# Kernel optimization log

Hardware: AMD Instinct MI355X
Metric: run time of the kernel (lower is better)

The kernel has to match this reference:

```python
import jax, jax.numpy as jnp
import numpy as np

N = 100000
E = 1600000
N_FEAT = 128
H1 = 256
H2 = 32
N_CLASS = 16


def spmm(row, col, vals, x):
    # sparse [N,N] @ dense [N,d]: gather source rows, scale by edge value,
    # scatter-add into destination rows.
    return jax.ops.segment_sum(vals[:, None] * x[col], row, num_segments=N)


def setup_inputs() -> dict:
    key = jax.random.key(0)
    ks = jax.random.split(key, 12)
    x_in = jax.random.normal(ks[0], (N, N_FEAT), dtype=jnp.float32)
    adj_row = jax.random.randint(ks[1], (E,), 0, N, dtype=jnp.int64)
    adj_col = jax.random.randint(ks[2], (E,), 0, N, dtype=jnp.int64)
    adj_vals = jax.random.uniform(ks[3], (E,), dtype=jnp.float32)
    s1 = 1.0 / np.sqrt(N_FEAT)
    s2 = 1.0 / np.sqrt(H1)
    s3 = 1.0 / np.sqrt(H2)
    W1 = jax.random.uniform(ks[4], (N_FEAT, H1), jnp.float32, -s1, s1)
    b1 = jax.random.uniform(ks[5], (H1,), jnp.float32, -s1, s1)
    W2 = jax.random.uniform(ks[6], (H1, H2), jnp.float32, -s2, s2)
    b2 = jax.random.uniform(ks[7], (H2,), jnp.float32, -s2, s2)
    W3 = jax.random.uniform(ks[8], (H2, N_CLASS), jnp.float32, -s3, s3)
    b3 = jax.random.uniform(ks[9], (N_CLASS,), jnp.float32, -s3, s3)
    return {"x_in": x_in, "adj_row": adj_row, "adj_col": adj_col,
            "adj_vals": adj_vals, "W1": W1, "b1": b1, "W2": W2, "b2": b2,
            "W3": W3, "b3": b3}


def reference(x_in, adj_row, adj_col, adj_vals, W1, b1, W2, b2, W3, b3):
    # layer 1: ReLU(Linear(adj @ x)); dropout is identity at inference
    h = jax.nn.relu(spmm(adj_row, adj_col, adj_vals, x_in) @ W1 + b1)
    # layer 2: ReLU(Linear(adj @ h))
    t = jax.nn.relu(spmm(adj_row, adj_col, adj_vals, h) @ W2 + b2)
    logits = t @ W3 + b3
    return jax.nn.log_softmax(logits, axis=1), t
```

## Files before the change

### kernel.cpp

```cpp
#include <hip/hip_runtime.h>
#include <hip/hip_bf16.h>

#define NN 100000
#define NE 1600000
#define NF 128
#define NH1 256
#define NH2 32
#define NC 16

#define NB 196
#define BSH 9
#define NCHUNK 512
#define CHSZ (NE / NCHUNK)

typedef __attribute__((ext_vector_type(4))) float f32x4;
typedef __attribute__((ext_vector_type(8))) short s16x8;
typedef __attribute__((ext_vector_type(4))) short s16x4;

__device__ __forceinline__ unsigned short f2bu(float f) {
    union { float f; unsigned u; } v; v.f = f;
    unsigned r = v.u + 0x7FFFu + ((v.u >> 16) & 1u);
    return (unsigned short)(r >> 16);
}
__device__ __forceinline__ float bflo(unsigned w) { return __uint_as_float(w << 16); }
__device__ __forceinline__ float bfhi(unsigned w) { return __uint_as_float(w & 0xFFFF0000u); }

__device__ __forceinline__ int detect_st(const int* arow) {
    const unsigned* a = (const unsigned*)arow;
    unsigned acc = 0;
#pragma unroll
    for (int i = 1; i < 32; i += 2) acc |= a[i];
    return acc == 0u ? 2 : 1;
}

__global__ __launch_bounds__(256) void fat0_k(const float* __restrict__ x, short* __restrict__ xb,
                                              const float* __restrict__ W1, const float* __restrict__ W2,
                                              short* __restrict__ w1t, short* __restrict__ w2t,
                                              const int* __restrict__ arow, int* __restrict__ histc) {
    int bid = blockIdx.x;
    if (bid < NCHUNK) {
        __shared__ int h[NB];
        for (int j = threadIdx.x; j < NB; j += 256) h[j] = 0;
        __syncthreads();
        int st = detect_st(arow);
        int base = bid * CHSZ;
        for (int i = base + threadIdx.x; i < base + CHSZ; i += 256)
            atomicAdd(&h[arow[(size_t)i * st] >> BSH], 1);
        __syncthreads();
        for (int j = threadIdx.x; j < NB; j += 256) histc[bid * NB + j] = h[j];
    } else if (bid < NCHUNK + 1024) {
        const int total = NN * NF / 4;
        for (int i = (bid - NCHUNK) * 256 + threadIdx.x; i < total; i += 1024 * 256) {
            f32x4 v = ((const f32x4*)x)[i];
            s16x4 o;
            for (int j = 0; j < 4; ++j) o[j] = (short)f2bu(v[j]);
            ((s16x4*)xb)[i] = o;
        }
    } else {
        int i = (bid - NCHUNK - 1024) * 256 + threadIdx.x;
        if (i < NF * NH1) {
            int k = i / NH1, c = i % NH1;
            w1t[c * NF + k] = (short)f2bu(W1[i]);
        } else {
            int j = i - NF * NH1;
            if (j < NH1 * NH2) {
                int k = j / NH2, c = j % NH2;
                w2t[c * NH1 + k] = (short)f2bu(W2[j]);
            }
        }
    }
}

__global__ __launch_bounds__(256) void scanb_k(const int* __restrict__ histc,
                                               int* __restrict__ cur,
                                               int* __restrict__ totals) {
    __shared__ int s[256];
    int b = blockIdx.x, t = threadIdx.x;
    int v0 = histc[(2 * t) * NB + b], v1 = histc[(2 * t + 1) * NB + b];
    int sum = v0 + v1;
    s[t] = sum; __syncthreads();
    for (int off = 1; off < 256; off <<= 1) {
        int u = (t >= off) ? s[t - off] : 0;
        __syncthreads();
        s[t] += u;
        __syncthreads();
    }
    int excl = s[t] - sum;
    cur[(2 * t) * NB + b] = excl;
    cur[(2 * t + 1) * NB + b] = excl + v0;
    if (t == 255) totals[b] = s[255];
}

__global__ __launch_bounds__(256) void scat_k(const int* __restrict__ arow,
                                              const int* __restrict__ acol,
                                              const float* __restrict__ avals,
                                              const int* __restrict__ totals,
                                              const int* __restrict__ cur,
                                              uint2* __restrict__ recs) {
    __shared__ int lcur[NB];
    __shared__ int ss[256];
    int t = threadIdx.x;
    int tv = (t < NB) ? totals[t] : 0;
    ss[t] = tv; __syncthreads();
    for (int off = 1; off < 256; off <<= 1) {
        int u = (t >= off) ? ss[t - off] : 0;
        __syncthreads();
        ss[t] += u;
        __syncthreads();
    }
    if (t < NB) lcur[t] = (ss[t] - tv) + cur[blockIdx.x * NB + t];
    __syncthreads();
    int st = detect_st(arow);
    int base = blockIdx.x * CHSZ;
    for (int i = base + t; i < base + CHSZ; i += 256) {
        int r   = arow[(size_t)i * st];
        int col = acol[(size_t)i * st];
        float v = avals[i];
        int b = r >> BSH;
        int p = atomicAdd(&lcur[b], 1);
        uint2 rec;
        rec.x = (unsigned)col | ((unsigned)(r & 511) << 17);
        rec.y = __float_as_uint(v);
        recs[p] = rec;
    }
}

__global__ __launch_bounds__(256) void sortb_k(const uint2* __restrict__ recs,
                                               const int* __restrict__ totals,
                                               int* __restrict__ rptr,
                                               uint2* __restrict__ epack) {
    __shared__ int hist[512], cur[512], sc[256], ss[256];
    __shared__ int s0sh, s1sh;
    int b = blockIdx.x, t = threadIdx.x;
    int tv = (t < NB) ? totals[t] : 0;
    ss[t] = tv; __syncthreads();
    for (int off = 1; off < 256; off <<= 1) {
        int u = (t >= off) ? ss[t - off] : 0;
        __syncthreads();
        ss[t] += u;
        __syncthreads();
    }
    if (t == b) { s0sh = ss[t] - tv; s1sh = ss[t]; }
    for (int j = t; j < 512; j += 256) hist[j] = 0;
    __syncthreads();
    int s0 = s0sh, s1 = s1sh;
    for (int i = s0 + t; i < s1; i += 256)
        atomicAdd(&hist[(recs[i].x >> 17) & 511], 1);
    __syncthreads();
    int v0 = hist[2 * t], v1 = hist[2 * t + 1], sum = v0 + v1;
    sc[t] = sum; __syncthreads();
    for (int off = 1; off < 256; off <<= 1) {
        int u = (t >= off) ? sc[t - off] : 0;
        __syncthreads();
        sc[t] += u;
        __syncthreads();
    }
    int excl = sc[t] - sum;
    cur[2 * t] = excl; cur[2 * t + 1] = excl + v0;
    __syncthreads();
    int nrows = NN - b * 512; if (nrows > 512) nrows = 512;
    for (int j = t; j < nrows; j += 256) rptr[b * 512 + j] = s0 + cur[j];
    if (b == 0 && t == 0) rptr[NN] = NE;
    __syncthreads();
    for (int i = s0 + t; i < s1; i += 256) {
        uint2 rc = recs[i];
        int rl = (rc.x >> 17) & 511;
        int p = s0 + atomicAdd(&cur[rl], 1);
        uint2 ep;
        ep.x = rc.x & 0x1FFFF;
        ep.y = rc.y;
        epack[p] = ep;
    }
}

__global__ __launch_bounds__(256) void spmm1_k(const int* __restrict__ rptr,
                                               const uint2* __restrict__ ep,
                                               const short* __restrict__ xb,
                                               short* __restrict__ agg1) {
    int row = blockIdx.x * 4 + (threadIdx.x >> 6);
    if (row >= NN) return;
    int lane = threadIdx.x & 63;
    int q = lane >> 4, f = lane & 15;
    int s = rptr[row], e = rptr[row + 1];
    float acc[8] = {};
    int i = s + q;
    for (; i + 4 < e; i += 8) {
        uint2 m0 = ep[i];
        uint2 m1 = ep[i + 4];
        uint4 g0 = *(const uint4*)&xb[(size_t)m0.x * NF + f * 8];
        uint4 g1 = *(const uint4*)&xb[(size_t)m1.x * NF + f * 8];
        float v0 = __uint_as_float(m0.y);
        float v1 = __uint_as_float(m1.y);
        acc[0] += v0 * bflo(g0.x); acc[1] += v0 * bfhi(g0.x);
        acc[2] += v0 * bflo(g0.y); acc[3] += v0 * bfhi(g0.y);
        acc[4] += v0 * bflo(g0.z); acc[5] += v0 * bfhi(g0.z);
        acc[6] += v0 * bflo(g0.w); acc[7] += v0 * bfhi(g0.w);
        acc[0] += v1 * bflo(g1.x); acc[1] += v1 * bfhi(g1.x);
        acc[2] += v1 * bflo(g1.y); acc[3] += v1 * bfhi(g1.y);
        acc[4] += v1 * bflo(g1.z); acc[5] += v1 * bfhi(g1.z);
        acc[6] += v1 * bflo(g1.w); acc[7] += v1 * bfhi(g1.w);
    }
    if (i < e) {
        uint2 m = ep[i];
        uint4 g = *(const uint4*)&xb[(size_t)m.x * NF + f * 8];
        float v = __uint_as_float(m.y);
        acc[0] += v * bflo(g.x); acc[1] += v * bfhi(g.x);
        acc[2] += v * bflo(g.y); acc[3] += v * bfhi(g.y);
        acc[4] += v * bflo(g.z); acc[5] += v * bfhi(g.z);
        acc[6] += v * bflo(g.w); acc[7] += v * bfhi(g.w);
    }
#pragma unroll
    for (int j = 0; j < 8; ++j) {
        acc[j] += __shfl_xor(acc[j], 16, 64);
        acc[j] += __shfl_xor(acc[j], 32, 64);
    }
    if (q == 0) {
        uint4 o4;
        o4.x = ((unsigned)f2bu(acc[1]) << 16) | f2bu(acc[0]);
        o4.y = ((unsigned)f2bu(acc[3]) << 16) | f2bu(acc[2]);
        o4.z = ((unsigned)f2bu(acc[5]) << 16) | f2bu(acc[4]);
        o4.w = ((unsigned)f2bu(acc[7]) << 16) | f2bu(acc[6]);
        *(uint4*)&agg1[(size_t)row * NF + f * 8] = o4;
    }
}

__global__ __launch_bounds__(256) void gemm12_k(const short* __restrict__ agg1,
                                                const short* __restrict__ w1t,
                                                const float* __restrict__ b1,
                                                const short* __restrict__ w2t,
                                                short* __restrict__ hw) {
    __shared__ char lds[87040];
    short* a_s  = (short*)lds;
    short* w_s  = (short*)(lds + 17408);
    short* h_s  = (short*)lds;
    short* w2_s = (short*)(lds + 33792);
    int tid = threadIdx.x;
    int r0 = blockIdx.x * 64;
    {
        int row = tid >> 2, kk = (tid & 3) * 32, gr = r0 + row;
        for (int i = 0; i < 4; ++i) {
            int k = kk + i * 8;
            s16x8 v = {};
            if (gr < NN) v = *(const s16x8*)&agg1[(size_t)gr * NF + k];
            *(s16x8*)&a_s[row * 136 + k] = v;
        }
    }
    {
        for (int i = 0; i < 16; ++i) {
            int k = i * 8;
            *(s16x8*)&w_s[tid * 136 + k] = *(const s16x8*)&w1t[(size_t)tid * NF + k];
        }
    }
    __syncthreads();
    int w = tid >> 6, l = tid & 63, lr = l & 15, hi = l >> 4;
    f32x4 acc[4][4] = {};
    for (int ks = 0; ks < 4; ++ks) {
        int kb = ks * 32 + hi * 8;
        s16x8 ar[4], br[4];
        for (int mi = 0; mi < 4; ++mi) ar[mi] = *(const s16x8*)&a_s[(mi * 16 + lr) * 136 + kb];
        for (int nj = 0; nj < 4; ++nj) br[nj] = *(const s16x8*)&w_s[(w * 64 + nj * 16 + lr) * 136 + kb];
        for (int mi = 0; mi < 4; ++mi)
            for (int nj = 0; nj < 4; ++nj)
                acc[mi][nj] = __builtin_amdgcn_mfma_f32_16x16x32_bf16(ar[mi], br[nj], acc[mi][nj], 0, 0, 0);
    }
    float bias[4];
    for (int nj = 0; nj < 4; ++nj) bias[nj] = b1[w * 64 + nj * 16 + lr];
    __syncthreads();
    for (int mi = 0; mi < 4; ++mi) {
        int rr = mi * 16 + hi * 4;
        for (int nj = 0; nj < 4; ++nj) {
            int cc = w * 64 + nj * 16 + lr;
            for (int q = 0; q < 4; ++q) {
                float v = acc[mi][nj][q] + bias[nj];
                v = v > 0.f ? v : 0.f;
                h_s[(rr + q) * 264 + cc] = (short)f2bu(v);
            }
        }
    }
    {
        int c = tid >> 3, kk = (tid & 7) * 32;
        for (int i = 0; i < 4; ++i) {
            int k = kk + i * 8;
            *(s16x8*)&w2_s[c * 264 + k] = *(const s16x8*)&w2t[(size_t)c * NH1 + k];
        }
    }
    __syncthreads();
    f32x4 acc2[2] = {};
    for (int ks = 0; ks < 8; ++ks) {
        int kb = ks * 32 + hi * 8;
        s16x8 ar = *(const s16x8*)&h_s[(w * 16 + lr) * 264 + kb];
        for (int nj = 0; nj < 2; ++nj) {
            s16x8 br = *(const s16x8*)&w2_s[(nj * 16 + lr) * 264 + kb];
            acc2[nj] = __builtin_amdgcn_mfma_f32_16x16x32_bf16(ar, br, acc2[nj], 0, 0, 0);
        }
    }
    for (int nj = 0; nj < 2; ++nj) {
        int c = nj * 16 + lr;
        for (int q = 0; q < 4; ++q) {
            int r = r0 + w * 16 + hi * 4 + q;
            if (r < NN) hw[(size_t)r * NH2 + c] = (short)f2bu(acc2[nj][q]);
        }
    }
}

__global__ __launch_bounds__(256) void spmm2_k(const int* __restrict__ rptr,
                                               const uint2* __restrict__ ep,
                                               const short* __restrict__ hw,
                                               const float* __restrict__ b2,
                                               float* __restrict__ t_out) {
    int row = blockIdx.x * 4 + (threadIdx.x >> 6);
    if (row >= NN) return;
    int lane = threadIdx.x & 63;
    int o = lane >> 3, f = lane & 7;
    int s = rptr[row], e = rptr[row + 1];
    float a0 = 0.f, a1 = 0.f, a2 = 0.f, a3 = 0.f;
    int i = s + o;
    for (; i + 8 < e; i += 16) {
        uint2 m0 = ep[i], m1 = ep[i + 8];
        uint2 g0 = *(const uint2*)&hw[(size_t)m0.x * NH2 + f * 4];
        uint2 g1 = *(const uint2*)&hw[(size_t)m1.x * NH2 + f * 4];
        float v0 = __uint_as_float(m0.y), v1 = __uint_as_float(m1.y);
        a0 += v0 * bflo(g0.x); a1 += v0 * bfhi(g0.x);
        a2 += v0 * bflo(g0.y); a3 += v0 * bfhi(g0.y);
        a0 += v1 * bflo(g1.x); a1 += v1 * bfhi(g1.x);
        a2 += v1 * bflo(g1.y); a3 += v1 * bfhi(g1.y);
    }
    if (i < e) {
        uint2 m = ep[i];
        uint2 g = *(const uint2*)&hw[(size_t)m.x * NH2 + f * 4];
        float v = __uint_as_float(m.y);
        a0 += v * bflo(g.x); a1 += v * bfhi(g.x);
        a2 += v * bflo(g.y); a3 += v * bfhi(g.y);
    }
    a0 += __shfl_xor(a0, 8, 64); a0 += __shfl_xor(a0, 16, 64); a0 += __shfl_xor(a0, 32, 64);
    a1 += __shfl_xor(a1, 8, 64); a1 += __shfl_xor(a1, 16, 64); a1 += __shfl_xor(a1, 32, 64);
    a2 += __shfl_xor(a2, 8, 64); a2 += __shfl_xor(a2, 16, 64); a2 += __shfl_xor(a2, 32, 64);
    a3 += __shfl_xor(a3, 8, 64); a3 += __shfl_xor(a3, 16, 64); a3 += __shfl_xor(a3, 32, 64);
    if (o == 0) {
        f32x4 ov;
        float r0 = a0 + b2[f * 4];
        float r1 = a1 + b2[f * 4 + 1];
        float r2 = a2 + b2[f * 4 + 2];
        float r3 = a3 + b2[f * 4 + 3];
        ov[0] = r0 > 0.f ? r0 : 0.f;
        ov[1] = r1 > 0.f ? r1 : 0.f;
        ov[2] = r2 > 0.f ? r2 : 0.f;
        ov[3] = r3 > 0.f ? r3 : 0.f;
        *(f32x4*)&t_out[(size_t)row * NH2 + f * 4] = ov;
    }
}

__global__ __launch_bounds__(256) void gemm3_k(const float* __restrict__ t_in,
                                               const float* __restrict__ W3,
                                               const float* __restrict__ b3,
                                               float* __restrict__ out) {
    __shared__ float t_s[256 * 33];
    __shared__ float w3s[NH2 * NC];
    __shared__ float b3s[NC];
    int tid = threadIdx.x;
    int r0 = blockIdx.x * 256;
    for (int j = 0; j < 32; ++j) {
        int flat = tid + j * 256;
        int r = flat >> 5, k = flat & 31;
        int gr = r0 + r;
        t_s[r * 33 + k] = (gr < NN) ? t_in[(size_t)gr * NH2 + k] : 0.f;
    }
    for (int j = tid; j < NH2 * NC; j += 256) w3s[j] = W3[j];
    if (tid < NC) b3s[tid] = b3[tid];
    __syncthreads();
    int gr = r0 + tid;
    if (gr >= NN) return;
    float lg[NC];
    for (int c = 0; c < NC; ++c) lg[c] = b3s[c];
    for (int k = 0; k < NH2; ++k) {
        float a = t_s[tid * 33 + k];
        for (int c = 0; c < NC; ++c) lg[c] += a * w3s[k * NC + c];
    }
    float m = lg[0];
    for (int c = 1; c < NC; ++c) m = fmaxf(m, lg[c]);
    float s = 0.f;
    for (int c = 0; c < NC; ++c) s += expf(lg[c] - m);
    float lo = logf(s) + m;
    f32x4* po = (f32x4*)&out[(size_t)gr * NC];
    for (int c4 = 0; c4 < 4; ++c4) {
        f32x4 v;
        for (int q = 0; q < 4; ++q) v[q] = lg[c4 * 4 + q] - lo;
        po[c4] = v;
    }
}

extern "C" void kernel_launch(void* const* d_in, const int* in_sizes, int n_in,
                              void* d_out, int out_size, void* d_ws, size_t ws_size,
                              hipStream_t stream) {
    const float* x_in  = (const float*)d_in[0];
    const int*   arow  = (const int*)d_in[1];
    const int*   acol  = (const int*)d_in[2];
    const float* avals = (const float*)d_in[3];
    const float* W1    = (const float*)d_in[4];
    const float* b1    = (const float*)d_in[5];
    const float* W2    = (const float*)d_in[6];
    const float* b2    = (const float*)d_in[7];
    const float* W3    = (const float*)d_in[8];
    const float* b3    = (const float*)d_in[9];
    float* out = (float*)d_out;
    float* t_out = out + (size_t)NN * NC;

    char* p = (char*)d_ws;
    size_t o = 0;
    auto alloc = [&](size_t bytes) -> void* {
        void* r = p + o;
        o += (bytes + 255) & ~(size_t)255;
        return r;
    };
    uint2* recs  = (uint2*)alloc((size_t)NE * 8);
    uint2* epack = (uint2*)alloc((size_t)NE * 8);
    int*   histc = (int*)  alloc((size_t)NCHUNK * NB * 4);
    int*   cur   = (int*)  alloc((size_t)NCHUNK * NB * 4);
    int*   totals= (int*)  alloc((size_t)NB * 4);
    int*   rptr  = (int*)  alloc((size_t)(NN + 1) * 4);
    short* w1t   = (short*)alloc((size_t)NF * NH1 * 2);
    short* w2t   = (short*)alloc((size_t)NH1 * NH2 * 2);
    short* xb    = (short*)alloc((size_t)NN * NF * 2);
    short* agg1  = (short*)alloc((size_t)NN * NF * 2);
    short* hw    = (short*)alloc((size_t)NN * NH2 * 2);

    fat0_k<<<NCHUNK + 1024 + 160, 256, 0, stream>>>(x_in, xb, W1, W2, w1t, w2t, arow, histc);
    scanb_k<<<NB, 256, 0, stream>>>(histc, cur, totals);
    scat_k<<<NCHUNK, 256, 0, stream>>>(arow, acol, avals, totals, cur, recs);
    sortb_k<<<NB, 256, 0, stream>>>(recs, totals, rptr, epack);
    spmm1_k<<<25000, 256, 0, stream>>>(rptr, epack, xb, agg1);
    gemm12_k<<<1563, 256, 0, stream>>>(agg1, w1t, b1, w2t, hw);
    spmm2_k<<<25000, 256, 0, stream>>>(rptr, epack, hw, b2, t_out);
    gemm3_k<<<391, 256, 0, stream>>>(t_out, W3, b3, out);
}
```

Before: 210.7 us.

## Stage scatter records in LDS by bin and halve gemm12 W1 LDS footprint

The scatter kernel now computes each chunk's per-bin local offsets with a second prefix scan over its histogram. It stages records in shared memory grouped by bucket, then writes them out in contiguous order per bin, so the global stores are more coalesced than the earlier random scattered writes. gemm12 loads W1 in two 128-column passes into a smaller LDS buffer, cutting LDS use from about 87KB to 52KB. That should let more blocks fit per CU, at the cost of an extra barrier and W1 reload per block. MAC8/MAC4 macros are a cleanup only.

```diff
diff --git a/kernel.cpp b/kernel.cpp
--- a/kernel.cpp
+++ b/kernel.cpp
@@ -95,11 +95,15 @@
                                               const int* __restrict__ acol,
                                               const float* __restrict__ avals,
                                               const int* __restrict__ totals,
+                                              const int* __restrict__ histc,
                                               const int* __restrict__ cur,
                                               uint2* __restrict__ recs) {
-    __shared__ int lcur[NB];
+    __shared__ uint2 stage[CHSZ];
+    __shared__ int desti[CHSZ];
+    __shared__ int gb[NB];
+    __shared__ int bincur[NB];
     __shared__ int ss[256];
-    int t = threadIdx.x;
+    int c = blockIdx.x, t = threadIdx.x;
     int tv = (t < NB) ? totals[t] : 0;
     ss[t] = tv; __syncthreads();
     for (int off = 1; off < 256; off <<= 1) {
@@ -108,21 +112,37 @@
         ss[t] += u;
         __syncthreads();
     }
-    if (t < NB) lcur[t] = (ss[t] - tv) + cur[blockIdx.x * NB + t];
+    int bstart = ss[t] - tv;
+    if (t < NB) gb[t] = bstart + cur[c * NB + t];
+    __syncthreads();
+    int hv = (t < NB) ? histc[c * NB + t] : 0;
+    ss[t] = hv; __syncthreads();
+    for (int off = 1; off < 256; off <<= 1) {
+        int u = (t >= off) ? ss[t - off] : 0;
+        __syncthreads();
+        ss[t] += u;
+        __syncthreads();
+    }
+    int boff = ss[t] - hv;
+    if (t < NB) { bincur[t] = boff; gb[t] -= boff; }
     __syncthreads();
     int st = detect_st(arow);
-    int base = blockIdx.x * CHSZ;
+    int base = c * CHSZ;
     for (int i = base + t; i < base + CHSZ; i += 256) {
         int r   = arow[(size_t)i * st];
         int col = acol[(size_t)i * st];
         float v = avals[i];
         int b = r >> BSH;
-        int p = atomicAdd(&lcur[b], 1);
+        int p = atomicAdd(&bincur[b], 1);
         uint2 rec;
         rec.x = (unsigned)col | ((unsigned)(r & 511) << 17);
         rec.y = __float_as_uint(v);
-        recs[p] = rec;
-    }
+        stage[p] = rec;
+        desti[p] = gb[b] + p;
+    }
+    __syncthreads();
+    for (int j = t; j < CHSZ; j += 256)
+        recs[desti[j]] = stage[j];
 }
 
 __global__ __launch_bounds__(256) void sortb_k(const uint2* __restrict__ recs,
@@ -172,6 +192,12 @@
         epack[p] = ep;
     }
 }
+
+#define MAC8(g, v) do { \
+    acc[0] += (v) * bflo(g.x); acc[1] += (v) * bfhi(g.x); \
+    acc[2] += (v) * bflo(g.y); acc[3] += (v) * bfhi(g.y); \
+    acc[4] += (v) * bflo(g.z); acc[5] += (v) * bfhi(g.z); \
+    acc[6] += (v) * bflo(g.w); acc[7] += (v) * bfhi(g.w); } while (0)
 
 __global__ __launch_bounds__(256) void spmm1_k(const int* __restrict__ rptr,
                                                const uint2* __restrict__ ep,
@@ -191,23 +217,13 @@
         uint4 g1 = *(const uint4*)&xb[(size_t)m1.x * NF + f * 8];
         float v0 = __uint_as_float(m0.y);
         float v1 = __uint_as_float(m1.y);
-        acc[0] += v0 * bflo(g0.x); acc[1] += v0 * bfhi(g0.x);
-        acc[2] += v0 * bflo(g0.y); acc[3] += v0 * bfhi(g0.y);
-        acc[4] += v0 * bflo(g0.z); acc[5] += v0 * bfhi(g0.z);
-        acc[6] += v0 * bflo(g0.w); acc[7] += v0 * bfhi(g0.w);
-        acc[0] += v1 * bflo(g1.x); acc[1] += v1 * bfhi(g1.x);
-        acc[2] += v1 * bflo(g1.y); acc[3] += v1 * bfhi(g1.y);
-        acc[4] += v1 * bflo(g1.z); acc[5] += v1 * bfhi(g1.z);
-        acc[6] += v1 * bflo(g1.w); acc[7] += v1 * bfhi(g1.w);
+        MAC8(g0, v0); MAC8(g1, v1);
     }
     if (i < e) {
         uint2 m = ep[i];
         uint4 g = *(const uint4*)&xb[(size_t)m.x * NF + f * 8];
         float v = __uint_as_float(m.y);
-        acc[0] += v * bflo(g.x); acc[1] += v * bfhi(g.x);
-        acc[2] += v * bflo(g.y); acc[3] += v * bfhi(g.y);
-        acc[4] += v * bflo(g.z); acc[5] += v * bfhi(g.z);
-        acc[6] += v * bflo(g.w); acc[7] += v * bfhi(g.w);
+        MAC8(g, v);
     }
 #pragma unroll
     for (int j = 0; j < 8; ++j) {
@@ -229,13 +245,14 @@
                                                 const float* __restrict__ b1,
                                                 const short* __restrict__ w2t,
                                                 short* __restrict__ hw) {
-    __shared__ char lds[87040];
+    __shared__ char lds[52224];
     short* a_s  = (short*)lds;
-    short* w_s  = (short*)(lds + 17408);
+    short* wt_s = (short*)(lds + 17408);
     short* h_s  = (short*)lds;
     short* w2_s = (short*)(lds + 33792);
     int tid = threadIdx.x;
     int r0 = blockIdx.x * 64;
+    int w = tid >> 6, l = tid & 63, lr = l & 15, hi = l >> 4;
     {
         int row = tid >> 2, kk = (tid & 3) * 32, gr = r0 + row;
         for (int i = 0; i < 4; ++i) {
@@ -245,38 +262,43 @@
             *(s16x8*)&a_s[row * 136 + k] = v;
         }
     }
-    {
-        for (int i = 0; i < 16; ++i) {
-            int k = i * 8;
-            *(s16x8*)&w_s[tid * 136 + k] = *(const s16x8*)&w1t[(size_t)tid * NF + k];
-        }
-    }
-    __syncthreads();
-    int w = tid >> 6, l = tid & 63, lr = l & 15, hi = l >> 4;
-    f32x4 acc[4][4] = {};
-    for (int ks = 0; ks < 4; ++ks) {
-        int kb = ks * 32 + hi * 8;
-        s16x8 ar[4], br[4];
-        for (int mi = 0; mi < 4; ++mi) ar[mi] = *(const s16x8*)&a_s[(mi * 16 + lr) * 136 + kb];
-        for (int nj = 0; nj < 4; ++nj) br[nj] = *(const s16x8*)&w_s[(w * 64 + nj * 16 + lr) * 136 + kb];
-        for (int mi = 0; mi < 4; ++mi)
-            for (int nj = 0; nj < 4; ++nj)
-                acc[mi][nj] = __builtin_amdgcn_mfma_f32_16x16x32_bf16(ar[mi], br[nj], acc[mi][nj], 0, 0, 0);
-    }
-    float bias[4];
-    for (int nj = 0; nj < 4; ++nj) bias[nj] = b1[w * 64 + nj * 16 + lr];
-    __syncthreads();
-    for (int mi = 0; mi < 4; ++mi) {
-        int rr = mi * 16 + hi * 4;
-        for (int nj = 0; nj < 4; ++nj) {
-            int cc = w * 64 + nj * 16 + lr;
-            for (int q = 0; q < 4; ++q) {
-                float v = acc[mi][nj][q] + bias[nj];
-                v = v > 0.f ? v : 0.f;
-                h_s[(rr + q) * 264 + cc] = (short)f2bu(v);
+    f32x4 acc[2][4][2] = {};
+    for (int pass = 0; pass < 2; ++pass) {
+        if (pass) __syncthreads();
+        {
+            int cl = tid >> 1, kk = (tid & 1) * 64;
+            const short* src = &w1t[(size_t)(pass * 128 + cl) * NF + kk];
+            for (int i = 0; i < 8; ++i)
+                *(s16x8*)&wt_s[cl * 136 + kk + i * 8] = *(const s16x8*)&src[i * 8];
+        }
+        __syncthreads();
+        for (int ks = 0; ks < 4; ++ks) {
+            int kb = ks * 32 + hi * 8;
+            s16x8 ar[4], br[2];
+            for (int mi = 0; mi < 4; ++mi) ar[mi] = *(const s16x8*)&a_s[(mi * 16 + lr) * 136 + kb];
+            for (int nj = 0; nj < 2; ++nj) br[nj] = *(const s16x8*)&wt_s[(w * 32 + nj * 16 + lr) * 136 + kb];
+            for (int mi = 0; mi < 4; ++mi)
+                for (int nj = 0; nj < 2; ++nj)
+                    acc[pass][mi][nj] = __builtin_amdgcn_mfma_f32_16x16x32_bf16(ar[mi], br[nj], acc[pass][mi][nj], 0, 0, 0);
+        }
+    }
+    float bias[2][2];
+    for (int pass = 0; pass < 2; ++pass)
+        for (int nj = 0; nj < 2; ++nj)
+            bias[pass][nj] = b1[pass * 128 + w * 32 + nj * 16 + lr];
+    __syncthreads();
+    for (int pass = 0; pass < 2; ++pass)
+        for (int mi = 0; mi < 4; ++mi) {
+            int rr = mi * 16 + hi * 4;
+            for (int nj = 0; nj < 2; ++nj) {
+                int cc = pass * 128 + w * 32 + nj * 16 + lr;
+                for (int q = 0; q < 4; ++q) {
+                    float v = acc[pass][mi][nj][q] + bias[pass][nj];
+                    v = v > 0.f ? v : 0.f;
+                    h_s[(rr + q) * 264 + cc] = (short)f2bu(v);
+                }
             }
         }
-    }
     {
         int c = tid >> 3, kk = (tid & 7) * 32;
         for (int i = 0; i < 4; ++i) {
@@ -302,6 +324,10 @@
         }
     }
 }
+
+#define MAC4(g, v) do { \
+    a0 += (v) * bflo(g.x); a1 += (v) * bfhi(g.x); \
+    a2 += (v) * bflo(g.y); a3 += (v) * bfhi(g.y); } while (0)
 
 __global__ __launch_bounds__(256) void spmm2_k(const int* __restrict__ rptr,
                                                const uint2* __restrict__ ep,
@@ -320,17 +346,13 @@
         uint2 g0 = *(const uint2*)&hw[(size_t)m0.x * NH2 + f * 4];
         uint2 g1 = *(const uint2*)&hw[(size_t)m1.x * NH2 + f * 4];
         float v0 = __uint_as_float(m0.y), v1 = __uint_as_float(m1.y);
-        a0 += v0 * bflo(g0.x); a1 += v0 * bfhi(g0.x);
-        a2 += v0 * bflo(g0.y); a3 += v0 * bfhi(g0.y);
-        a0 += v1 * bflo(g1.x); a1 += v1 * bfhi(g1.x);
-        a2 += v1 * bflo(g1.y); a3 += v1 * bfhi(g1.y);
+        MAC4(g0, v0); MAC4(g1, v1);
     }
     if (i < e) {
         uint2 m = ep[i];
         uint2 g = *(const uint2*)&hw[(size_t)m.x * NH2 + f * 4];
         float v = __uint_as_float(m.y);
-        a0 += v * bflo(g.x); a1 += v * bfhi(g.x);
-        a2 += v * bflo(g.y); a3 += v * bfhi(g.y);
+        MAC4(g, v);
     }
     a0 += __shfl_xor(a0, 8, 64); a0 += __shfl_xor(a0, 16, 64); a0 += __shfl_xor(a0, 32, 64);
     a1 += __shfl_xor(a1, 8, 64); a1 += __shfl_xor(a1, 16, 64); a1 += __shfl_xor(a1, 32, 64);
@@ -426,7 +448,7 @@
 
     fat0_k<<<NCHUNK + 1024 + 160, 256, 0, stream>>>(x_in, xb, W1, W2, w1t, w2t, arow, histc);
     scanb_k<<<NB, 256, 0, stream>>>(histc, cur, totals);
-    scat_k<<<NCHUNK, 256, 0, stream>>>(arow, acol, avals, totals, cur, recs);
+    scat_k<<<NCHUNK, 256, 0, stream>>>(arow, acol, avals, totals, histc, cur, recs);
     sortb_k<<<NB, 256, 0, stream>>>(recs, totals, rptr, epack);
     spmm1_k<<<25000, 256, 0, stream>>>(rptr, epack, xb, agg1);
     gemm12_k<<<1563, 256, 0, stream>>>(agg1, w1t, b1, w2t, hw);
```

New measurement: 198.9 us. 5.6% less time.
